# Performance work log

Hardware: AMD Instinct MI355X
Metric: run time of the kernel (lower is better)

## Reference

```python
import jax, jax.numpy as jnp
import numpy as np

B, L, S, H, E = 4, 1024, 1024, 8, 64
MASK_SCALE = 10000.0
TAU_MIN, TAU_MAX = 0.1, 5.0
TH_MIN, TH_MAX = 0.01, 0.99
EPS = 1e-8


def setup_inputs() -> dict:
    k0 = jax.random.key(0)
    ks = jax.random.split(k0, 5)
    query = jax.random.normal(ks[0], (B, L, H, E), jnp.float32)
    key = jax.random.normal(ks[1], (B, S, H, E), jnp.float32)
    value = jax.random.normal(ks[2], (B, S, H, E), jnp.float32)
    # positions: monotone per batch -> standard causal mask
    pos = jnp.arange(B * L, dtype=jnp.float32).reshape(B, L, 1)
    phi = jax.random.normal(ks[3], (H, L, S), jnp.float32)
    # uniform noise for Gumbel-sigmoid reparameterization (torch.rand_like)
    u = jax.random.uniform(ks[4], (H, L, S), jnp.float32)
    log_tau = jnp.asarray(np.log(2.0), jnp.float32)
    threshold = jnp.asarray(0.5, jnp.float32)
    return {"query": query, "key": key, "value": value, "pos": pos,
            "phi": phi, "u": u, "log_tau": log_tau, "threshold": threshold,
            "causal_mask": 1}


def reference(query, key, value, pos, phi, u, log_tau, threshold, causal_mask):
    Bq, Lq, Hq, Eq = query.shape
    scale = 1.0 / np.sqrt(Eq).astype(np.float32)
    # raw attention scores (B,H,L,S)
    scores = jnp.einsum('blhe,bshe->bhls', query, key)
    if causal_mask:
        p = pos[..., 0]                       # (B,L)
        # M[b,i,j] = -inf where p[b,j] > p[b,i]
        neg_inf = jnp.asarray(-jnp.inf, scores.dtype)
        M = jnp.where(p[:, None, :] > p[:, :, None], neg_inf, 0.0)  # (B,L,S)
        scores = scores + M[:, None, :, :]
    # learnable DAG mask via Gumbel-sigmoid relaxation
    tau = jnp.clip(jnp.exp(log_tau), TAU_MIN, TAU_MAX)
    gumbel = jnp.log(u + EPS) - jnp.log(1.0 - u + EPS)
    m_relaxed = jax.nn.sigmoid((gumbel + phi) / tau)      # (H,L,S)
    thresh = jnp.clip(threshold, TH_MIN, TH_MAX)
    phi_mask = -MASK_SCALE * jax.nn.relu(thresh - m_relaxed)
    scores = scores + phi_mask[None]                      # broadcast over batch
    att = jax.nn.softmax(scale * scores, axis=-1)          # (B,H,L,S)
    # per-query attention entropy (B,H,L)
    entropy = -jnp.sum(att * jnp.log(jnp.clip(att, EPS, None)), axis=-1)
    entropy = jnp.nan_to_num(entropy, nan=0.0)
    # dropout p=0 (eval) -> A = att
    V = jnp.einsum('bhls,bshd->blhd', att, value)          # (B,L,H,E)
    return V, att, entropy
```

## Files before the change

kernel.cpp:

```cpp
#include <hip/hip_runtime.h>

#define BN 4
#define LN 1024
#define SN 1024
#define HN 8
#define EN 64
#define OFF_ATT (BN * LN * HN * EN)
#define OFF_ENT (OFF_ATT + BN * HN * LN * SN)

#define WS_MW 0u
#define WS_KB 16777216u
#define WS_VT (WS_KB + 4194304u)

#define APITCH 2064

typedef __attribute__((ext_vector_type(8))) __bf16 bf16x8;
typedef __attribute__((ext_vector_type(4))) float f32x4;
typedef __attribute__((ext_vector_type(4))) unsigned int uint4v;
typedef __attribute__((ext_vector_type(2))) unsigned int uint2v;
typedef __attribute__((ext_vector_type(4))) _Float16 f16x4;

__device__ __forceinline__ void decode_block(int x, int& b, int& lb) {
  int lbLo = x & 7;
  b = (x >> 3) & 3;
  lb = (x >> 5) * 8 + lbLo;
}

__device__ __forceinline__ void cvt8(const float* p, uint4v& hv, uint4v& lv) {
  float4 a = *(const float4*)p;
  float4 bq = *(const float4*)(p + 4);
  float x[8] = {a.x, a.y, a.z, a.w, bq.x, bq.y, bq.z, bq.w};
  unsigned int h[8], lo[8];
#pragma unroll
  for (int i = 0; i < 8; ++i) {
    unsigned int ub = __float_as_uint(x[i]);
    h[i] = ub >> 16;
    float lf = x[i] - __uint_as_float(ub & 0xffff0000u);
    lo[i] = __float_as_uint(lf) >> 16;
  }
  hv = uint4v{h[0] | (h[1] << 16), h[2] | (h[3] << 16),
              h[4] | (h[5] << 16), h[6] | (h[7] << 16)};
  lv = uint4v{lo[0] | (lo[1] << 16), lo[2] | (lo[3] << 16),
              lo[4] | (lo[5] << 16), lo[6] | (lo[7] << 16)};
}

__device__ __forceinline__ uint4v pack8_trunc(float4 a, float4 b) {
  return uint4v{(__float_as_uint(a.x) >> 16) | (__float_as_uint(a.y) & 0xffff0000u),
                (__float_as_uint(a.z) >> 16) | (__float_as_uint(a.w) & 0xffff0000u),
                (__float_as_uint(b.x) >> 16) | (__float_as_uint(b.y) & 0xffff0000u),
                (__float_as_uint(b.z) >> 16) | (__float_as_uint(b.w) & 0xffff0000u)};
}

__global__ __launch_bounds__(256) void k_prep(
    const float* __restrict__ kk, const float* __restrict__ vv,
    const float* __restrict__ phi, const float* __restrict__ u,
    const float* __restrict__ p_logtau, const float* __restrict__ p_thresh,
    _Float16* __restrict__ mw, unsigned short* __restrict__ kb,
    unsigned short* __restrict__ vT) {
  const int bx = blockIdx.x;
  if (bx < 8192) {
    const float tau = fminf(fmaxf(__expf(p_logtau[0]), 0.1f), 5.0f);
    const float rtau = 1.0f / tau;
    const float thr = fminf(fmaxf(p_thresh[0], 0.01f), 0.99f);
    int idx = (bx * 256 + threadIdx.x) * 4;
    float4 u4 = *(const float4*)(u + idx);
    float4 p4 = *(const float4*)(phi + idx);
    float uu[4] = {u4.x, u4.y, u4.z, u4.w};
    float pp[4] = {p4.x, p4.y, p4.z, p4.w};
    f16x4 o;
#pragma unroll
    for (int i = 0; i < 4; ++i) {
      float g = __logf(__fdividef(uu[i] + 1e-8f, 1.0f - uu[i] + 1e-8f));
      float z = (g + pp[i]) * rtau;
      float sig = __fdividef(1.0f, 1.0f + __expf(-z));
      o[i] = (_Float16)(-10000.0f * fmaxf(thr - sig, 0.0f) * 0.125f);
    }
    *(f16x4*)(mw + idx) = o;
  } else if (bx < 9216) {
    int gid = (bx - 8192) * 256 + threadIdx.x;
    int e8 = gid & 7;
    int tmp = gid >> 3;
    int h = tmp & 7;
    int bs = tmp >> 3;
    int s = bs & 1023;
    int b = bs >> 10;
    const float* src = kk + (size_t)gid * 8;
    float4 a = *(const float4*)src;
    float4 bq = *(const float4*)(src + 4);
    *(uint4v*)(kb + (((size_t)(b * 8 + h) * 1024 + s) * 64) + e8 * 8) =
        pack8_trunc(a, bq);
  } else {
    int gid = (bx - 9216) * 256 + threadIdx.x;
    int s8 = gid & 127;
    int t1 = gid >> 7;
    int e = t1 & 63;
    int t2 = t1 >> 6;
    int h = t2 & 7;
    int b = t2 >> 3;
    float x[8];
#pragma unroll
    for (int j = 0; j < 8; ++j)
      x[j] = vv[((size_t)(b * 1024 + s8 * 8 + j) * 8 + h) * 64 + e];
    uint4v pv = pack8_trunc(float4{x[0], x[1], x[2], x[3]},
                            float4{x[4], x[5], x[6], x[7]});
    *(uint4v*)(vT + ((size_t)(b * 8 + h) * 64 + e) * 1024 + s8 * 8) = pv;
  }
}

__global__ __launch_bounds__(512, 4) void k_fused(
    const float* __restrict__ q, const unsigned short* __restrict__ kb,
    const unsigned short* __restrict__ vT, const _Float16* __restrict__ mw,
    const int* __restrict__ p_causal, float* __restrict__ out) {
  int b, lb;
  decode_block(blockIdx.x, b, lb);
  const int h = blockIdx.y;
  const int tid = threadIdx.x;
  const int w = __builtin_amdgcn_readfirstlane(tid >> 6);
  const int c = tid & 63;
  const int cl = c & 15;
  const int cg = c >> 4;

  __shared__ __align__(16) unsigned char lds_att[32 * APITCH];
  __shared__ float red0[8][16], redZ[8][16], redE[8][16];

  const int causal = p_causal[0];
  const unsigned short* kbb = kb + ((size_t)(b * 8 + h) * 1024) * 64;

  {
    const unsigned char* gmask =
        (const unsigned char*)(mw + ((size_t)h * LN + lb * 32) * SN);
    uint4v mk[8];
#pragma unroll
    for (int i = 0; i < 8; ++i)
      mk[i] = *(const uint4v*)(gmask + i * 8192 + tid * 16);
#pragma unroll
    for (int i = 0; i < 8; ++i) {
      int goff = i * 8192 + tid * 16;
      *(uint4v*)(lds_att + (goff >> 11) * APITCH + (goff & 2047)) = mk[i];
    }
  }
  __syncthreads();

#pragma unroll
  for (int qt = 0; qt < 2; ++qt) {
    const int l = lb * 32 + qt * 16 + cl;

    uint4v qh[2], ql[2];
#pragma unroll
    for (int cc = 0; cc < 2; ++cc) {
      const float* qp = q + (((size_t)b * LN + l) * HN + h) * EN + cc * 32 + cg * 8;
      cvt8(qp, qh[cc], ql[cc]);
    }

    f32x4 accs[8];
#pragma unroll
    for (int tgb = 0; tgb < 2; ++tgb) {
      uint4v kf[4][2];
#pragma unroll
      for (int t2 = 0; t2 < 4; ++t2)
#pragma unroll
        for (int cc = 0; cc < 2; ++cc)
          kf[t2][cc] = *(const uint4v*)(kbb +
                                        (size_t)(w * 128 + (tgb * 4 + t2) * 16 + cl) * 64 +
                                        cc * 32 + cg * 8);
#pragma unroll
      for (int t2 = 0; t2 < 4; ++t2) {
        f32x4 acc = f32x4{0.f, 0.f, 0.f, 0.f};
#pragma unroll
        for (int cc = 0; cc < 2; ++cc) {
          bf16x8 kv = __builtin_bit_cast(bf16x8, kf[t2][cc]);
          acc = __builtin_amdgcn_mfma_f32_16x16x32_bf16(
              kv, __builtin_bit_cast(bf16x8, qh[cc]), acc, 0, 0, 0);
          acc = __builtin_amdgcn_mfma_f32_16x16x32_bf16(
              kv, __builtin_bit_cast(bf16x8, ql[cc]), acc, 0, 0, 0);
        }
        accs[tgb * 4 + t2] = acc;
      }
    }

    const unsigned char* mrow = lds_att + (qt * 16 + cl) * APITCH;
    float mx = -3.0e38f;
#pragma unroll
    for (int tg = 0; tg < 8; ++tg) {
      const int s0 = w * 128 + tg * 16 + cg * 4;
      f16x4 m4 = *(const f16x4*)(mrow + s0 * 2);
#pragma unroll
      for (int r = 0; r < 4; ++r) {
        float v = fmaf(accs[tg][r], 0.125f, (float)m4[r]);
        bool maskd = (causal != 0) && (s0 + r > l);
        v = maskd ? -1.0e30f : v;
        accs[tg][r] = v;
        mx = fmaxf(mx, v);
      }
    }
    mx = fmaxf(mx, __shfl_xor(mx, 16, 64));
    mx = fmaxf(mx, __shfl_xor(mx, 32, 64));
    if (cg == 0) red0[w][cl] = mx;
    __syncthreads();
    float bmx = red0[0][cl];
#pragma unroll
    for (int i = 1; i < 8; ++i) bmx = fmaxf(bmx, red0[i][cl]);

    float zz = 0.f, ee = 0.f;
#pragma unroll
    for (int tg = 0; tg < 8; ++tg) {
#pragma unroll
      for (int r = 0; r < 4; ++r) {
        float tt = accs[tg][r] - bmx;
        float ex = __expf(tt);
        zz += ex;
        ee = fmaf(ex, fmaxf(tt, -88.0f), ee);
        accs[tg][r] = ex;
      }
    }
    zz += __shfl_xor(zz, 16, 64);
    zz += __shfl_xor(zz, 32, 64);
    ee += __shfl_xor(ee, 16, 64);
    ee += __shfl_xor(ee, 32, 64);
    if (cg == 0) { redZ[w][cl] = zz; redE[w][cl] = ee; }
    __syncthreads();
    float Z = redZ[0][cl], E = redE[0][cl];
#pragma unroll
    for (int i = 1; i < 8; ++i) { Z += redZ[i][cl]; E += redE[i][cl]; }
    const float rz = __fdividef(1.0f, Z);
    if (w == 0 && cg == 0)
      out[OFF_ENT + ((size_t)b * HN + h) * LN + l] = __logf(Z) - E * rz;

    unsigned char* arow = lds_att + (qt * 16 + cl) * APITCH;
#pragma unroll
    for (int tg = 0; tg < 8; ++tg) {
      const int s0 = w * 128 + tg * 16 + cg * 4;
      float ax = accs[tg][0] * rz, ay = accs[tg][1] * rz;
      float az = accs[tg][2] * rz, aw = accs[tg][3] * rz;
      uint2v pk = uint2v{
          (__float_as_uint(ax) >> 16) | (__float_as_uint(ay) & 0xffff0000u),
          (__float_as_uint(az) >> 16) | (__float_as_uint(aw) & 0xffff0000u)};
      *(uint2v*)(arow + s0 * 2) = pk;
    }
  }

  const int et = w & 3, sh = w >> 2;
  const unsigned short* vbb =
      vT + ((size_t)(b * 8 + h) * 64 + et * 16 + cl) * 1024 + sh * 512;
  uint4v vf0[8];
#pragma unroll
  for (int j = 0; j < 8; ++j)
    vf0[j] = *(const uint4v*)(vbb + j * 32 + cg * 8);

  __syncthreads();

  {
    float* abase = out + OFF_ATT + (((size_t)b * HN + h) * LN + lb * 32) * SN;
#pragma unroll
    for (int rr = 0; rr < 4; ++rr) {
      const int row = w * 4 + rr;
      const unsigned char* src = lds_att + row * APITCH;
      float* dst = abase + (size_t)row * SN;
#pragma unroll
      for (int it = 0; it < 4; ++it) {
        uint2v pk = *(const uint2v*)(src + it * 512 + c * 8);
        f32x4 o = f32x4{__uint_as_float(pk.x << 16),
                        __uint_as_float(pk.x & 0xffff0000u),
                        __uint_as_float(pk.y << 16),
                        __uint_as_float(pk.y & 0xffff0000u)};
        __builtin_nontemporal_store(o, (f32x4*)(dst + it * 256 + c * 4));
      }
    }
  }

  f32x4 acc00 = f32x4{0.f, 0.f, 0.f, 0.f}, acc01 = f32x4{0.f, 0.f, 0.f, 0.f};
  f32x4 acc10 = f32x4{0.f, 0.f, 0.f, 0.f}, acc11 = f32x4{0.f, 0.f, 0.f, 0.f};
#pragma unroll
  for (int scb = 0; scb < 2; ++scb) {
    uint4v vf[8];
    if (scb == 0) {
#pragma unroll
      for (int j = 0; j < 8; ++j) vf[j] = vf0[j];
    } else {
#pragma unroll
      for (int j = 0; j < 8; ++j)
        vf[j] = *(const uint4v*)(vbb + 256 + j * 32 + cg * 8);
    }
#pragma unroll
    for (int qt = 0; qt < 2; ++qt) {
      uint4v af[8];
#pragma unroll
      for (int j = 0; j < 8; ++j)
        af[j] = *(const uint4v*)(lds_att + (qt * 16 + cl) * APITCH +
                                 (sh * 512 + scb * 256 + j * 32 + cg * 8) * 2);
#pragma unroll
      for (int j = 0; j < 8; ++j) {
        bf16x8 a8 = __builtin_bit_cast(bf16x8, vf[j]);
        bf16x8 b8 = __builtin_bit_cast(bf16x8, af[j]);
        if (qt == 0) {
          if (j & 1)
            acc01 = __builtin_amdgcn_mfma_f32_16x16x32_bf16(a8, b8, acc01, 0, 0, 0);
          else
            acc00 = __builtin_amdgcn_mfma_f32_16x16x32_bf16(a8, b8, acc00, 0, 0, 0);
        } else {
          if (j & 1)
            acc11 = __builtin_amdgcn_mfma_f32_16x16x32_bf16(a8, b8, acc11, 0, 0, 0);
          else
            acc10 = __builtin_amdgcn_mfma_f32_16x16x32_bf16(a8, b8, acc10, 0, 0, 0);
        }
      }
    }
  }
  f32x4 sum0 = acc00 + acc01;
  f32x4 sum1 = acc10 + acc11;

  __syncthreads();

  *(f32x4*)(lds_att + cl * APITCH + sh * 1024 + (et * 16 + cg * 4) * 4) = sum0;
  *(f32x4*)(lds_att + (16 + cl) * APITCH + sh * 1024 + (et * 16 + cg * 4) * 4) = sum1;

  __syncthreads();

  {
    const int r = tid >> 4, e4 = tid & 15;
    f32x4 p0 = *(const f32x4*)(lds_att + r * APITCH + e4 * 16);
    f32x4 p1 = *(const f32x4*)(lds_att + r * APITCH + 1024 + e4 * 16);
    f32x4 s = p0 + p1;
    float* dst = out + (((size_t)b * LN + lb * 32 + r) * HN + h) * EN + e4 * 4;
    __builtin_nontemporal_store(s, (f32x4*)dst);
  }
}

extern "C" void kernel_launch(void* const* d_in, const int* in_sizes, int n_in,
                              void* d_out, int out_size, void* d_ws, size_t ws_size,
                              hipStream_t stream) {
  (void)in_sizes; (void)n_in; (void)out_size; (void)ws_size;
  const float* q   = (const float*)d_in[0];
  const float* k   = (const float*)d_in[1];
  const float* v   = (const float*)d_in[2];
  const float* phi = (const float*)d_in[4];
  const float* u   = (const float*)d_in[5];
  const float* lt  = (const float*)d_in[6];
  const float* th  = (const float*)d_in[7];
  const int*   cm  = (const int*)d_in[8];
  float* out = (float*)d_out;

  _Float16* mw = (_Float16*)((char*)d_ws + WS_MW);
  unsigned short* kb = (unsigned short*)((char*)d_ws + WS_KB);
  unsigned short* vT = (unsigned short*)((char*)d_ws + WS_VT);

  k_prep<<<dim3(10240), dim3(256), 0, stream>>>(k, v, phi, u, lt, th, mw, kb, vT);
  k_fused<<<dim3(128, 8, 1), dim3(512), 0, stream>>>(q, kb, vT, mw, cm, out);
}
```

Before: 104.2 us.

## Drop split-bf16 Q, round to nearest, batch both query tiles per barrier

Q is now rounded once to bf16 with round-to-nearest-even instead of being split into high and low bf16 halves. This halves the QK^T MFMA count. K, V and the attention probabilities also switch from truncation to RNE rounding to limit the lost accuracy. Both 16-row query tiles are now computed up front and their max and sum reductions share barriers, cutting the __syncthreads count from four to two. The cost is lower score precision, more live accumulator registers (16 f32x4), and removal of the -88 clamp in the entropy term.

```diff
diff --git a/kernel.cpp b/kernel.cpp
--- a/kernel.cpp
+++ b/kernel.cpp
@@ -26,29 +26,15 @@
   lb = (x >> 5) * 8 + lbLo;
 }
 
-__device__ __forceinline__ void cvt8(const float* p, uint4v& hv, uint4v& lv) {
-  float4 a = *(const float4*)p;
-  float4 bq = *(const float4*)(p + 4);
-  float x[8] = {a.x, a.y, a.z, a.w, bq.x, bq.y, bq.z, bq.w};
-  unsigned int h[8], lo[8];
-#pragma unroll
-  for (int i = 0; i < 8; ++i) {
-    unsigned int ub = __float_as_uint(x[i]);
-    h[i] = ub >> 16;
-    float lf = x[i] - __uint_as_float(ub & 0xffff0000u);
-    lo[i] = __float_as_uint(lf) >> 16;
-  }
-  hv = uint4v{h[0] | (h[1] << 16), h[2] | (h[3] << 16),
-              h[4] | (h[5] << 16), h[6] | (h[7] << 16)};
-  lv = uint4v{lo[0] | (lo[1] << 16), lo[2] | (lo[3] << 16),
-              lo[4] | (lo[5] << 16), lo[6] | (lo[7] << 16)};
-}
-
-__device__ __forceinline__ uint4v pack8_trunc(float4 a, float4 b) {
-  return uint4v{(__float_as_uint(a.x) >> 16) | (__float_as_uint(a.y) & 0xffff0000u),
-                (__float_as_uint(a.z) >> 16) | (__float_as_uint(a.w) & 0xffff0000u),
-                (__float_as_uint(b.x) >> 16) | (__float_as_uint(b.y) & 0xffff0000u),
-                (__float_as_uint(b.z) >> 16) | (__float_as_uint(b.w) & 0xffff0000u)};
+__device__ __forceinline__ unsigned int rne2(float x, float y) {
+  unsigned int ux = __float_as_uint(x), uy = __float_as_uint(y);
+  ux += 0x7fffu + ((ux >> 16) & 1u);
+  uy += 0x7fffu + ((uy >> 16) & 1u);
+  return (ux >> 16) | (uy & 0xffff0000u);
+}
+
+__device__ __forceinline__ uint4v pack8_rne(float4 a, float4 b) {
+  return uint4v{rne2(a.x, a.y), rne2(a.z, a.w), rne2(b.x, b.y), rne2(b.z, b.w)};
 }
 
 __global__ __launch_bounds__(256) void k_prep(
@@ -88,7 +74,7 @@
     float4 a = *(const float4*)src;
     float4 bq = *(const float4*)(src + 4);
     *(uint4v*)(kb + (((size_t)(b * 8 + h) * 1024 + s) * 64) + e8 * 8) =
-        pack8_trunc(a, bq);
+        pack8_rne(a, bq);
   } else {
     int gid = (bx - 9216) * 256 + threadIdx.x;
     int s8 = gid & 127;
@@ -101,8 +87,8 @@
 #pragma unroll
     for (int j = 0; j < 8; ++j)
       x[j] = vv[((size_t)(b * 1024 + s8 * 8 + j) * 8 + h) * 64 + e];
-    uint4v pv = pack8_trunc(float4{x[0], x[1], x[2], x[3]},
-                            float4{x[4], x[5], x[6], x[7]});
+    uint4v pv = pack8_rne(float4{x[0], x[1], x[2], x[3]},
+                          float4{x[4], x[5], x[6], x[7]});
     *(uint4v*)(vT + ((size_t)(b * 8 + h) * 64 + e) * 1024 + s8 * 8) = pv;
   }
 }
@@ -121,7 +107,7 @@
   const int cg = c >> 4;
 
   __shared__ __align__(16) unsigned char lds_att[32 * APITCH];
-  __shared__ float red0[8][16], redZ[8][16], redE[8][16];
+  __shared__ float red0[2][8][16], redZ[2][8][16], redE[2][8][16];
 
   const int causal = p_causal[0];
   const unsigned short* kbb = kb + ((size_t)(b * 8 + h) * 1024) * 64;
@@ -139,89 +125,103 @@
       *(uint4v*)(lds_att + (goff >> 11) * APITCH + (goff & 2047)) = mk[i];
     }
   }
-  __syncthreads();
-
+
+  uint4v qf[2][2];
+#pragma unroll
+  for (int qt = 0; qt < 2; ++qt)
+#pragma unroll
+    for (int cc = 0; cc < 2; ++cc) {
+      const float* qp = q + (((size_t)b * LN + lb * 32 + qt * 16 + cl) * HN + h) * EN +
+                        cc * 32 + cg * 8;
+      float4 a = *(const float4*)qp;
+      float4 bq = *(const float4*)(qp + 4);
+      qf[qt][cc] = pack8_rne(a, bq);
+    }
+
+  __syncthreads();
+
+  f32x4 accs[16];
+#pragma unroll
+  for (int tgb = 0; tgb < 2; ++tgb) {
+    uint4v kf[4][2];
+#pragma unroll
+    for (int t2 = 0; t2 < 4; ++t2)
+#pragma unroll
+      for (int cc = 0; cc < 2; ++cc)
+        kf[t2][cc] = *(const uint4v*)(kbb +
+                                      (size_t)(w * 128 + (tgb * 4 + t2) * 16 + cl) * 64 +
+                                      cc * 32 + cg * 8);
+#pragma unroll
+    for (int t2 = 0; t2 < 4; ++t2)
+#pragma unroll
+      for (int qt = 0; qt < 2; ++qt) {
+        f32x4 acc = f32x4{0.f, 0.f, 0.f, 0.f};
+#pragma unroll
+        for (int cc = 0; cc < 2; ++cc)
+          acc = __builtin_amdgcn_mfma_f32_16x16x32_bf16(
+              __builtin_bit_cast(bf16x8, kf[t2][cc]),
+              __builtin_bit_cast(bf16x8, qf[qt][cc]), acc, 0, 0, 0);
+        accs[qt * 8 + tgb * 4 + t2] = acc;
+      }
+  }
+
+  float mx[2] = {-3.0e38f, -3.0e38f};
 #pragma unroll
   for (int qt = 0; qt < 2; ++qt) {
     const int l = lb * 32 + qt * 16 + cl;
-
-    uint4v qh[2], ql[2];
-#pragma unroll
-    for (int cc = 0; cc < 2; ++cc) {
-      const float* qp = q + (((size_t)b * LN + l) * HN + h) * EN + cc * 32 + cg * 8;
-      cvt8(qp, qh[cc], ql[cc]);
-    }
-
-    f32x4 accs[8];
-#pragma unroll
-    for (int tgb = 0; tgb < 2; ++tgb) {
-      uint4v kf[4][2];
-#pragma unroll
-      for (int t2 = 0; t2 < 4; ++t2)
-#pragma unroll
-        for (int cc = 0; cc < 2; ++cc)
-          kf[t2][cc] = *(const uint4v*)(kbb +
-                                        (size_t)(w * 128 + (tgb * 4 + t2) * 16 + cl) * 64 +
-                                        cc * 32 + cg * 8);
-#pragma unroll
-      for (int t2 = 0; t2 < 4; ++t2) {
-        f32x4 acc = f32x4{0.f, 0.f, 0.f, 0.f};
-#pragma unroll
-        for (int cc = 0; cc < 2; ++cc) {
-          bf16x8 kv = __builtin_bit_cast(bf16x8, kf[t2][cc]);
-          acc = __builtin_amdgcn_mfma_f32_16x16x32_bf16(
-              kv, __builtin_bit_cast(bf16x8, qh[cc]), acc, 0, 0, 0);
-          acc = __builtin_amdgcn_mfma_f32_16x16x32_bf16(
-              kv, __builtin_bit_cast(bf16x8, ql[cc]), acc, 0, 0, 0);
-        }
-        accs[tgb * 4 + t2] = acc;
-      }
-    }
-
     const unsigned char* mrow = lds_att + (qt * 16 + cl) * APITCH;
-    float mx = -3.0e38f;
 #pragma unroll
     for (int tg = 0; tg < 8; ++tg) {
       const int s0 = w * 128 + tg * 16 + cg * 4;
       f16x4 m4 = *(const f16x4*)(mrow + s0 * 2);
 #pragma unroll
       for (int r = 0; r < 4; ++r) {
-        float v = fmaf(accs[tg][r], 0.125f, (float)m4[r]);
+        float v = fmaf(accs[qt * 8 + tg][r], 0.125f, (float)m4[r]);
         bool maskd = (causal != 0) && (s0 + r > l);
         v = maskd ? -1.0e30f : v;
-        accs[tg][r] = v;
-        mx = fmaxf(mx, v);
-      }
-    }
-    mx = fmaxf(mx, __shfl_xor(mx, 16, 64));
-    mx = fmaxf(mx, __shfl_xor(mx, 32, 64));
-    if (cg == 0) red0[w][cl] = mx;
-    __syncthreads();
-    float bmx = red0[0][cl];
-#pragma unroll
-    for (int i = 1; i < 8; ++i) bmx = fmaxf(bmx, red0[i][cl]);
-
-    float zz = 0.f, ee = 0.f;
+        accs[qt * 8 + tg][r] = v;
+        mx[qt] = fmaxf(mx[qt], v);
+      }
+    }
+    mx[qt] = fmaxf(mx[qt], __shfl_xor(mx[qt], 16, 64));
+    mx[qt] = fmaxf(mx[qt], __shfl_xor(mx[qt], 32, 64));
+    if (cg == 0) red0[qt][w][cl] = mx[qt];
+  }
+  __syncthreads();
+
+  float zz[2], ee[2];
+#pragma unroll
+  for (int qt = 0; qt < 2; ++qt) {
+    float bmx = red0[qt][0][cl];
+#pragma unroll
+    for (int i = 1; i < 8; ++i) bmx = fmaxf(bmx, red0[qt][i][cl]);
+    float z = 0.f, e = 0.f;
 #pragma unroll
     for (int tg = 0; tg < 8; ++tg) {
 #pragma unroll
       for (int r = 0; r < 4; ++r) {
-        float tt = accs[tg][r] - bmx;
+        float tt = accs[qt * 8 + tg][r] - bmx;
         float ex = __expf(tt);
-        zz += ex;
-        ee = fmaf(ex, fmaxf(tt, -88.0f), ee);
-        accs[tg][r] = ex;
-      }
-    }
-    zz += __shfl_xor(zz, 16, 64);
-    zz += __shfl_xor(zz, 32, 64);
-    ee += __shfl_xor(ee, 16, 64);
-    ee += __shfl_xor(ee, 32, 64);
-    if (cg == 0) { redZ[w][cl] = zz; redE[w][cl] = ee; }
-    __syncthreads();
-    float Z = redZ[0][cl], E = redE[0][cl];
-#pragma unroll
-    for (int i = 1; i < 8; ++i) { Z += redZ[i][cl]; E += redE[i][cl]; }
+        z += ex;
+        e = fmaf(ex, tt, e);
+        accs[qt * 8 + tg][r] = ex;
+      }
+    }
+    z += __shfl_xor(z, 16, 64);
+    z += __shfl_xor(z, 32, 64);
+    e += __shfl_xor(e, 16, 64);
+    e += __shfl_xor(e, 32, 64);
+    if (cg == 0) { redZ[qt][w][cl] = z; redE[qt][w][cl] = e; }
+    zz[qt] = z; ee[qt] = e;
+  }
+  __syncthreads();
+
+#pragma unroll
+  for (int qt = 0; qt < 2; ++qt) {
+    const int l = lb * 32 + qt * 16 + cl;
+    float Z = redZ[qt][0][cl], E = redE[qt][0][cl];
+#pragma unroll
+    for (int i = 1; i < 8; ++i) { Z += redZ[qt][i][cl]; E += redE[qt][i][cl]; }
     const float rz = __fdividef(1.0f, Z);
     if (w == 0 && cg == 0)
       out[OFF_ENT + ((size_t)b * HN + h) * LN + l] = __logf(Z) - E * rz;
@@ -230,11 +230,9 @@
 #pragma unroll
     for (int tg = 0; tg < 8; ++tg) {
       const int s0 = w * 128 + tg * 16 + cg * 4;
-      float ax = accs[tg][0] * rz, ay = accs[tg][1] * rz;
-      float az = accs[tg][2] * rz, aw = accs[tg][3] * rz;
-      uint2v pk = uint2v{
-          (__float_as_uint(ax) >> 16) | (__float_as_uint(ay) & 0xffff0000u),
-          (__float_as_uint(az) >> 16) | (__float_as_uint(aw) & 0xffff0000u)};
+      float ax = accs[qt * 8 + tg][0] * rz, ay = accs[qt * 8 + tg][1] * rz;
+      float az = accs[qt * 8 + tg][2] * rz, aw = accs[qt * 8 + tg][3] * rz;
+      uint2v pk = uint2v{rne2(ax, ay), rne2(az, aw)};
       *(uint2v*)(arow + s0 * 2) = pk;
     }
   }
```

Result: faster. 91.78 us (-11.9%).
